# Kernel tuning notes

Measured on AMD Instinct MI355X. Metric: run time of the kernel, lower is better.

## Reference

```python
import jax, jax.numpy as jnp
import numpy as np

NUM_LAYERS = 4
HIDDEN = 32
INPUT = 2
B = 16384
T = 64


def setup_inputs() -> dict:
    key = jax.random.key(0)
    ks = jax.random.split(key, 8)
    s = 1.0 / np.sqrt(HIDDEN)  # PyTorch LSTM default init scale
    return {
        "x": jax.random.normal(ks[0], (B, 3, T), dtype=jnp.float32),
        "W_ih0": jax.random.uniform(ks[1], (4 * HIDDEN, INPUT), minval=-s, maxval=s, dtype=jnp.float32),
        "W_ih": jax.random.uniform(ks[2], (NUM_LAYERS - 1, 4 * HIDDEN, HIDDEN), minval=-s, maxval=s, dtype=jnp.float32),
        "W_hh": jax.random.uniform(ks[3], (NUM_LAYERS, 4 * HIDDEN, HIDDEN), minval=-s, maxval=s, dtype=jnp.float32),
        "b_ih": jax.random.uniform(ks[4], (NUM_LAYERS, 4 * HIDDEN), minval=-s, maxval=s, dtype=jnp.float32),
        "b_hh": jax.random.uniform(ks[5], (NUM_LAYERS, 4 * HIDDEN), minval=-s, maxval=s, dtype=jnp.float32),
        "W_lin": jax.random.uniform(ks[6], (1, HIDDEN), minval=-s, maxval=s, dtype=jnp.float32),
        "b_lin": jax.random.uniform(ks[7], (1,), minval=-s, maxval=s, dtype=jnp.float32),
    }


def _lstm_cell(inp, h, c, Wih, Whh, b):
    # inp: [B, in_dim]; h, c: [B, H]; Wih: [4H, in_dim]; Whh: [4H, H]; b: [4H]
    gates = inp @ Wih.T + h @ Whh.T + b  # [B, 4H]
    i, f, g, o = jnp.split(gates, 4, axis=-1)  # PyTorch gate order: i, f, g, o
    i = jax.nn.sigmoid(i)
    f = jax.nn.sigmoid(f)
    g = jnp.tanh(g)
    o = jax.nn.sigmoid(o)
    c_new = f * c + i * g
    h_new = o * jnp.tanh(c_new)
    return h_new, c_new


def reference(x, W_ih0, W_ih, W_hh, b_ih, b_hh, W_lin, b_lin):
    # x: [B, 3, T]; channel 2 (id) is discarded, as in the original forward.
    feats = x[:, :2, :]                         # [B, 2, T]
    xs = jnp.transpose(feats, (2, 0, 1))        # [T, B, 2]
    bsz = x.shape[0]
    h0 = jnp.zeros((NUM_LAYERS, bsz, HIDDEN), dtype=x.dtype)
    c0 = jnp.zeros((NUM_LAYERS, bsz, HIDDEN), dtype=x.dtype)
    bias = b_ih + b_hh  # [L, 4H]

    def step(carry, xt):
        h, c = carry  # each [L, B, H]
        inp = xt
        hs, cs = [], []
        for l in range(NUM_LAYERS):
            Wih = W_ih0 if l == 0 else W_ih[l - 1]
            h_new, c_new = _lstm_cell(inp, h[l], c[l], Wih, W_hh[l], bias[l])
            hs.append(h_new)
            cs.append(c_new)
            inp = h_new
        return (jnp.stack(hs), jnp.stack(cs)), None

    (h, c), _ = jax.lax.scan(step, (h0, c0), xs)
    # last timestep's top-layer output -> linear -> sigmoid -> squeeze to [B]
    out = jax.nn.sigmoid(h[-1] @ W_lin.T + b_lin)  # [B, 1]
    return out.squeeze(-1)
```

## Files before the change

### kernel.cpp

```cpp
#include <hip/hip_runtime.h>

typedef float  f32x4  __attribute__((ext_vector_type(4)));
typedef short  bf16x8 __attribute__((ext_vector_type(8)));

#define TWOLOG2E   2.8853900817779268f
#define NLOG2E    -1.4426950408889634f
#define NTWOLOG2E -2.8853900817779268f

__device__ __forceinline__ unsigned short f2b(float f) {
    unsigned int u = __builtin_bit_cast(unsigned int, f);
    u += 0x7fffu + ((u >> 16) & 1u);
    return (unsigned short)(u >> 16);
}
__device__ __forceinline__ float b2f(unsigned short s) {
    unsigned int u = ((unsigned int)s) << 16;
    return __builtin_bit_cast(float, u);
}
__device__ __forceinline__ unsigned int pk2(float lo, float hi) {
#if __has_builtin(__builtin_amdgcn_cvt_pk_bf16_f32)
    typedef __bf16 bf16x2 __attribute__((ext_vector_type(2)));
    bf16x2 p = __builtin_amdgcn_cvt_pk_bf16_f32(lo, hi);
    return __builtin_bit_cast(unsigned int, p);
#else
    return (unsigned int)f2b(lo) | ((unsigned int)f2b(hi) << 16);
#endif
}
__device__ __forceinline__ float frcp(float x) { return __builtin_amdgcn_rcpf(x); }
__device__ __forceinline__ float fex2(float x) { return __builtin_amdgcn_exp2f(x); }

__global__ __launch_bounds__(256, 2)
void lstm_mfma(const float* __restrict__ xg,  const float* __restrict__ Wih0,
               const float* __restrict__ Wih, const float* __restrict__ Whh,
               const float* __restrict__ bih, const float* __restrict__ bhh,
               const float* __restrict__ Wlin,const float* __restrict__ blin,
               float* __restrict__ out) {
    __shared__ short        hb[16 * 1280] __attribute__((aligned(16)));
    __shared__ unsigned int xb[64 * 32];
    __shared__ int          prog[4];

    const int tid  = threadIdx.x;
    const int wv   = __builtin_amdgcn_readfirstlane(tid >> 6);
    const int lane = tid & 63;
    const int m    = lane & 15;
    const int q    = lane >> 4;
    const int row0 = blockIdx.x * 32;

    for (int i = tid; i < 10240; i += 256) ((unsigned int*)hb)[i] = 0u;
    if (tid < 4) prog[tid] = 0;

    for (int i = tid; i < 2048; i += 256) {
        int r = i >> 6, t = i & 63;
        float x0 = xg[(size_t)(row0 + r) * 192 + t];
        float x1 = xg[(size_t)(row0 + r) * 192 + 64 + t];
        xb[t * 32 + r] = pk2(x0, x1);
    }

    bf16x8 bfr[8][2];
    float  bv[8];
#pragma unroll
    for (int g = 0; g < 8; ++g) {
        const int   T    = g >> 1;
        const int   rowG = T * 32 + 2 * m + (g & 1);
        const float sc   = (T == 2) ? NTWOLOG2E : NLOG2E;
        bv[g] = (bih[wv * 128 + rowG] + bhh[wv * 128 + rowG]) * sc;
#pragma unroll
        for (int c = 0; c < 2; ++c) {
            const int k0 = c * 32 + q * 8;
            float w[8];
            if (wv == 0) {
                if (c == 0) {
#pragma unroll
                    for (int jj = 0; jj < 8; ++jj) w[jj] = 0.0f;
                    if (q == 0) { w[0] = Wih0[rowG * 2]; w[1] = Wih0[rowG * 2 + 1]; }
                } else {
                    const float* src = Whh + rowG * 32 + (k0 - 32);
#pragma unroll
                    for (int jj = 0; jj < 8; ++jj) w[jj] = src[jj];
                }
            } else {
                const float* src = (c == 0) ? (Wih + (wv - 1) * 4096 + rowG * 32 + k0)
                                            : (Whh + wv * 4096 + rowG * 32 + (k0 - 32));
#pragma unroll
                for (int jj = 0; jj < 8; ++jj) w[jj] = src[jj];
            }
            bf16x8 fr;
#pragma unroll
            for (int jj = 0; jj < 8; ++jj) fr[jj] = (short)f2b(w[jj] * sc);
            bfr[g][c] = fr;
        }
    }

    float cp[2][2][4];
#pragma unroll
    for (int tt = 0; tt < 2; ++tt)
#pragma unroll
        for (int hf = 0; hf < 2; ++hf)
#pragma unroll
            for (int r = 0; r < 4; ++r) cp[tt][hf][r] = 0.0f;

    __syncthreads();

    auto cell_step = [&](int t, const short* pa0, const short* pa1, short* hwr) {
        bf16x8 a0[2], a1[2];
#pragma unroll
        for (int tt = 0; tt < 2; ++tt) {
            if (wv == 0) {
                unsigned int xd = xb[t * 32 + tt * 16 + m];
                union { unsigned int u[4]; bf16x8 v; } au;
                au.u[0] = (q == 0) ? xd : 0u; au.u[1] = 0u; au.u[2] = 0u; au.u[3] = 0u;
                a0[tt] = au.v;
            } else {
                a0[tt] = *(const bf16x8*)(pa0 + (tt * 16 + m) * 40 + q * 8);
            }
            a1[tt] = *(const bf16x8*)(pa1 + (tt * 16 + m) * 40 + q * 8);
        }
#pragma unroll
        for (int tt = 0; tt < 2; ++tt) {
            f32x4 acc[8];
#pragma unroll
            for (int g = 0; g < 8; ++g) {
                f32x4 cb = {bv[g], bv[g], bv[g], bv[g]};
                acc[g] = __builtin_amdgcn_mfma_f32_16x16x32_bf16(a0[tt], bfr[g][0], cb, 0, 0, 0);
                acc[g] = __builtin_amdgcn_mfma_f32_16x16x32_bf16(a1[tt], bfr[g][1], acc[g], 0, 0, 0);
            }
            float h0[4];
#pragma unroll
            for (int hf = 0; hf < 2; ++hf) {
#pragma unroll
                for (int r = 0; r < 4; ++r) {
                    float ei = fex2(acc[0 + hf][r]);
                    float ef = fex2(acc[2 + hf][r]);
                    float eg = fex2(acc[4 + hf][r]);
                    float eo = fex2(acc[6 + hf][r]);
                    float ap_f = 1.0f + ef;
                    float p1   = (1.0f + ei) * (1.0f + eg);
                    float R_   = frcp(p1 * ap_f);
                    float egp  = __builtin_fmaf(eg, TWOLOG2E, NTWOLOG2E);
                    float t1   = egp * ap_f;
                    float t2   = __builtin_fmaf(cp[tt][hf][r], p1, t1);
                    float cn   = t2 * R_;
                    cp[tt][hf][r] = cn;
                    float ec = fex2(cn);
                    float Rh = frcp((1.0f + eo) * (1.0f + ec));
                    float hh = (1.0f - ec) * Rh;
                    if (hf == 0) h0[r] = hh;
                    else ((unsigned int*)hwr)[(tt * 16 + q * 4 + r) * 20 + m] = pk2(h0[r], hh);
                }
            }
        }
    };

    volatile int* vp = prog;
    short* const myBase = hb + wv * 4 * 1280;
    const short* const inBase = hb + (wv > 0 ? wv - 1 : 0) * 4 * 1280;

    for (int n = 0; n < 32; ++n) {
        if (wv > 0) { while (vp[wv - 1] < n + 1) __builtin_amdgcn_s_sleep(1); }
        if (wv < 3) { while (vp[wv + 1] < n - 1) __builtin_amdgcn_s_sleep(1); }
        asm volatile("" ::: "memory");

        const int t0 = 2 * n;
        const int s0 = t0 & 3, s1 = (t0 + 1) & 3, sr = (t0 + 3) & 3;
        short*       w0 = myBase + s0 * 1280;
        short*       w1 = myBase + s1 * 1280;
        const short* r0 = myBase + sr * 1280;
        const short* i0 = inBase + s0 * 1280;
        const short* i1 = inBase + s1 * 1280;

        cell_step(t0,     i0, r0, w0);
        cell_step(t0 + 1, i1, w0, w1);

        asm volatile("s_waitcnt lgkmcnt(0)" ::: "memory");
        if (lane == 0) vp[wv] = n + 1;
    }

    __syncthreads();

    if (tid < 32) {
        const short* h3 = hb + (3 * 4 + 3) * 1280 + tid * 40;
        float s = blin[0];
#pragma unroll
        for (int k = 0; k < 32; ++k)
            s += Wlin[k] * b2f((unsigned short)h3[k]);
        out[row0 + tid] = frcp(1.0f + fex2(s * NLOG2E));
    }
}

extern "C" void kernel_launch(void* const* d_in, const int* in_sizes, int n_in,
                              void* d_out, int out_size, void* d_ws, size_t ws_size,
                              hipStream_t stream) {
    const float* x    = (const float*)d_in[0];
    const float* Wih0 = (const float*)d_in[1];
    const float* Wih  = (const float*)d_in[2];
    const float* Whh  = (const float*)d_in[3];
    const float* bih  = (const float*)d_in[4];
    const float* bhh  = (const float*)d_in[5];
    const float* Wlin = (const float*)d_in[6];
    const float* blin = (const float*)d_in[7];
    float* out = (float*)d_out;

    lstm_mfma<<<512, 256, 0, stream>>>(x, Wih0, Wih, Whh, bih, bhh, Wlin, blin, out);
}
```

Before: 228.1 us.

## Replace layer-pipelined 4-wave blocks with single-wave blocks running all layers

Each block is now one wavefront that processes 16 batch rows and steps through all four LSTM layers one after another at every timestep. All layer weights stay in registers, and the hidden state is updated in place in a small LDS buffer. This removes the inter-wave progress flags, the spin-waits and the ring buffers of the old layer-pipelined scheme. In exchange it loses the overlap between layers and the two-tile ILP per wave, creates a longer serial dependency chain, and raises register pressure to roughly 256+ VGPRs, leaving about one wave per SIMD.

```diff
diff --git a/kernel.cpp b/kernel.cpp
--- a/kernel.cpp
+++ b/kernel.cpp
@@ -28,101 +28,104 @@
 __device__ __forceinline__ float frcp(float x) { return __builtin_amdgcn_rcpf(x); }
 __device__ __forceinline__ float fex2(float x) { return __builtin_amdgcn_exp2f(x); }
 
-__global__ __launch_bounds__(256, 2)
+__global__ __launch_bounds__(64, 1)
 void lstm_mfma(const float* __restrict__ xg,  const float* __restrict__ Wih0,
                const float* __restrict__ Wih, const float* __restrict__ Whh,
                const float* __restrict__ bih, const float* __restrict__ bhh,
                const float* __restrict__ Wlin,const float* __restrict__ blin,
                float* __restrict__ out) {
-    __shared__ short        hb[16 * 1280] __attribute__((aligned(16)));
-    __shared__ unsigned int xb[64 * 32];
-    __shared__ int          prog[4];
+    __shared__ short        hbuf[4 * 640] __attribute__((aligned(16)));
+    __shared__ unsigned int xb[64 * 16];
 
-    const int tid  = threadIdx.x;
-    const int wv   = __builtin_amdgcn_readfirstlane(tid >> 6);
-    const int lane = tid & 63;
+    const int lane = threadIdx.x;
     const int m    = lane & 15;
     const int q    = lane >> 4;
-    const int row0 = blockIdx.x * 32;
+    const int row0 = blockIdx.x * 16;
 
-    for (int i = tid; i < 10240; i += 256) ((unsigned int*)hb)[i] = 0u;
-    if (tid < 4) prog[tid] = 0;
+    for (int i = lane; i < 1280; i += 64) ((unsigned int*)hbuf)[i] = 0u;
 
-    for (int i = tid; i < 2048; i += 256) {
+    for (int i = lane; i < 1024; i += 64) {
         int r = i >> 6, t = i & 63;
         float x0 = xg[(size_t)(row0 + r) * 192 + t];
         float x1 = xg[(size_t)(row0 + r) * 192 + 64 + t];
-        xb[t * 32 + r] = pk2(x0, x1);
+        xb[t * 16 + r] = pk2(x0, x1);
     }
 
-    bf16x8 bfr[8][2];
-    float  bv[8];
+    bf16x8 bfr[4][8][2];
+    float  bv[4][8];
 #pragma unroll
-    for (int g = 0; g < 8; ++g) {
-        const int   T    = g >> 1;
-        const int   rowG = T * 32 + 2 * m + (g & 1);
-        const float sc   = (T == 2) ? NTWOLOG2E : NLOG2E;
-        bv[g] = (bih[wv * 128 + rowG] + bhh[wv * 128 + rowG]) * sc;
+    for (int l = 0; l < 4; ++l) {
 #pragma unroll
-        for (int c = 0; c < 2; ++c) {
-            const int k0 = c * 32 + q * 8;
-            float w[8];
-            if (wv == 0) {
-                if (c == 0) {
+        for (int g = 0; g < 8; ++g) {
+            const int   T    = g >> 1;
+            const int   rowG = T * 32 + 2 * m + (g & 1);
+            const float sc   = (T == 2) ? NTWOLOG2E : NLOG2E;
+            bv[l][g] = (bih[l * 128 + rowG] + bhh[l * 128 + rowG]) * sc;
 #pragma unroll
-                    for (int jj = 0; jj < 8; ++jj) w[jj] = 0.0f;
-                    if (q == 0) { w[0] = Wih0[rowG * 2]; w[1] = Wih0[rowG * 2 + 1]; }
+            for (int c = 0; c < 2; ++c) {
+                const int k0 = c * 32 + q * 8;
+                float w[8];
+                if (l == 0) {
+                    if (c == 0) {
+#pragma unroll
+                        for (int jj = 0; jj < 8; ++jj) w[jj] = 0.0f;
+                        if (q == 0) { w[0] = Wih0[rowG * 2]; w[1] = Wih0[rowG * 2 + 1]; }
+                    } else {
+                        const float* src = Whh + rowG * 32 + (k0 - 32);
+#pragma unroll
+                        for (int jj = 0; jj < 8; ++jj) w[jj] = src[jj];
+                    }
                 } else {
-                    const float* src = Whh + rowG * 32 + (k0 - 32);
+                    const float* src = (c == 0) ? (Wih + (l - 1) * 4096 + rowG * 32 + k0)
+                                                : (Whh + l * 4096 + rowG * 32 + (k0 - 32));
 #pragma unroll
                     for (int jj = 0; jj < 8; ++jj) w[jj] = src[jj];
                 }
-            } else {
-                const float* src = (c == 0) ? (Wih + (wv - 1) * 4096 + rowG * 32 + k0)
-                                            : (Whh + wv * 4096 + rowG * 32 + (k0 - 32));
+                bf16x8 fr;
 #pragma unroll
-                for (int jj = 0; jj < 8; ++jj) w[jj] = src[jj];
+                for (int jj = 0; jj < 8; ++jj) fr[jj] = (short)f2b(w[jj] * sc);
+                bfr[l][g][c] = fr;
             }
-            bf16x8 fr;
-#pragma unroll
-            for (int jj = 0; jj < 8; ++jj) fr[jj] = (short)f2b(w[jj] * sc);
-            bfr[g][c] = fr;
         }
     }
 
-    float cp[2][2][4];
+    float cp[4][2][4];
 #pragma unroll
-    for (int tt = 0; tt < 2; ++tt)
+    for (int l = 0; l < 4; ++l)
 #pragma unroll
         for (int hf = 0; hf < 2; ++hf)
 #pragma unroll
-            for (int r = 0; r < 4; ++r) cp[tt][hf][r] = 0.0f;
+            for (int r = 0; r < 4; ++r) cp[l][hf][r] = 0.0f;
 
     __syncthreads();
 
-    auto cell_step = [&](int t, const short* pa0, const short* pa1, short* hwr) {
-        bf16x8 a0[2], a1[2];
+    const int aoff = m * 40 + q * 8;
+
+    for (int t = 0; t < 64; ++t) {
 #pragma unroll
-        for (int tt = 0; tt < 2; ++tt) {
-            if (wv == 0) {
-                unsigned int xd = xb[t * 32 + tt * 16 + m];
+        for (int l = 0; l < 4; ++l) {
+            bf16x8 a1 = *(const bf16x8*)(hbuf + l * 640 + aoff);
+            bf16x8 a0;
+            if (l == 0) {
+                unsigned int xd = xb[t * 16 + m];
                 union { unsigned int u[4]; bf16x8 v; } au;
                 au.u[0] = (q == 0) ? xd : 0u; au.u[1] = 0u; au.u[2] = 0u; au.u[3] = 0u;
-                a0[tt] = au.v;
+                a0 = au.v;
             } else {
-                a0[tt] = *(const bf16x8*)(pa0 + (tt * 16 + m) * 40 + q * 8);
+                a0 = *(const bf16x8*)(hbuf + (l - 1) * 640 + aoff);
             }
-            a1[tt] = *(const bf16x8*)(pa1 + (tt * 16 + m) * 40 + q * 8);
-        }
-#pragma unroll
-        for (int tt = 0; tt < 2; ++tt) {
+
             f32x4 acc[8];
 #pragma unroll
             for (int g = 0; g < 8; ++g) {
-                f32x4 cb = {bv[g], bv[g], bv[g], bv[g]};
-                acc[g] = __builtin_amdgcn_mfma_f32_16x16x32_bf16(a0[tt], bfr[g][0], cb, 0, 0, 0);
-                acc[g] = __builtin_amdgcn_mfma_f32_16x16x32_bf16(a1[tt], bfr[g][1], acc[g], 0, 0, 0);
+                f32x4 cb = {bv[l][g], bv[l][g], bv[l][g], bv[l][g]};
+                acc[g] = __builtin_amdgcn_mfma_f32_16x16x32_bf16(a1, bfr[l][g][1], cb, 0, 0, 0);
             }
+#pragma unroll
+            for (int g = 0; g < 8; ++g)
+                acc[g] = __builtin_amdgcn_mfma_f32_16x16x32_bf16(a0, bfr[l][g][0], acc[g], 0, 0, 0);
+
+            unsigned int* hw = (unsigned int*)(hbuf + l * 640);
             float h0[4];
 #pragma unroll
             for (int hf = 0; hf < 2; ++hf) {
@@ -137,52 +140,26 @@
                     float R_   = frcp(p1 * ap_f);
                     float egp  = __builtin_fmaf(eg, TWOLOG2E, NTWOLOG2E);
                     float t1   = egp * ap_f;
-                    float t2   = __builtin_fmaf(cp[tt][hf][r], p1, t1);
+                    float t2   = __builtin_fmaf(cp[l][hf][r], p1, t1);
                     float cn   = t2 * R_;
-                    cp[tt][hf][r] = cn;
+                    cp[l][hf][r] = cn;
                     float ec = fex2(cn);
                     float Rh = frcp((1.0f + eo) * (1.0f + ec));
                     float hh = (1.0f - ec) * Rh;
                     if (hf == 0) h0[r] = hh;
-                    else ((unsigned int*)hwr)[(tt * 16 + q * 4 + r) * 20 + m] = pk2(h0[r], hh);
+                    else hw[(q * 4 + r) * 20 + m] = pk2(h0[r], hh);
                 }
             }
         }
-    };
-
-    volatile int* vp = prog;
-    short* const myBase = hb + wv * 4 * 1280;
-    const short* const inBase = hb + (wv > 0 ? wv - 1 : 0) * 4 * 1280;
-
-    for (int n = 0; n < 32; ++n) {
-        if (wv > 0) { while (vp[wv - 1] < n + 1) __builtin_amdgcn_s_sleep(1); }
-        if (wv < 3) { while (vp[wv + 1] < n - 1) __builtin_amdgcn_s_sleep(1); }
-        asm volatile("" ::: "memory");
-
-        const int t0 = 2 * n;
-        const int s0 = t0 & 3, s1 = (t0 + 1) & 3, sr = (t0 + 3) & 3;
-        short*       w0 = myBase + s0 * 1280;
-        short*       w1 = myBase + s1 * 1280;
-        const short* r0 = myBase + sr * 1280;
-        const short* i0 = inBase + s0 * 1280;
-        const short* i1 = inBase + s1 * 1280;
-
-        cell_step(t0,     i0, r0, w0);
-        cell_step(t0 + 1, i1, w0, w1);
-
-        asm volatile("s_waitcnt lgkmcnt(0)" ::: "memory");
-        if (lane == 0) vp[wv] = n + 1;
     }
 
-    __syncthreads();
-
-    if (tid < 32) {
-        const short* h3 = hb + (3 * 4 + 3) * 1280 + tid * 40;
+    if (lane < 16) {
+        const short* h3 = hbuf + 3 * 640 + lane * 40;
         float s = blin[0];
 #pragma unroll
         for (int k = 0; k < 32; ++k)
             s += Wlin[k] * b2f((unsigned short)h3[k]);
-        out[row0 + tid] = frcp(1.0f + fex2(s * NLOG2E));
+        out[row0 + lane] = frcp(1.0f + fex2(s * NLOG2E));
     }
 }
 
@@ -199,5 +176,5 @@
     const float* blin = (const float*)d_in[7];
     float* out = (float*)d_out;
 
-    lstm_mfma<<<512, 256, 0, stream>>>(x, Wih0, Wih, Whh, bih, bhh, Wlin, blin, out);
+    lstm_mfma<<<1024, 64, 0, stream>>>(x, Wih0, Wih, Whh, bih, bhh, Wlin, blin, out);
 }
```

After: 259.8 us. 13.9% more time.
